# Kernel optimization log

Hardware: AMD Instinct MI355X
Metric: run time of the kernel (lower is better)

Reference implementation:

```python
import jax, jax.numpy as jnp
import numpy as np

D_MODEL = 1024
N_HEADS = 16
D_K = D_MODEL // N_HEADS
ROPE_BASE = 10000.0


def _rope_tables(seq_len, dim, dtype=jnp.float32):
    # standard rotary: inv_freq over even dims, angles broadcast over positions
    inv_freq = 1.0 / (ROPE_BASE ** (jnp.arange(0, dim, 2, dtype=jnp.float32) / dim))
    t = jnp.arange(seq_len, dtype=jnp.float32)
    freqs = jnp.outer(t, inv_freq)                  # [S, dim/2]
    emb = jnp.concatenate([freqs, freqs], axis=-1)   # [S, dim]
    return jnp.cos(emb).astype(dtype), jnp.sin(emb).astype(dtype)


def _rotate_half(x):
    x1, x2 = jnp.split(x, 2, axis=-1)
    return jnp.concatenate([-x2, x1], axis=-1)


def _apply_rope(x, cos, sin):
    # x: [B, H, S, d_k]; cos/sin: [S, d_k]
    return x * cos[None, None, :, :] + _rotate_half(x) * sin[None, None, :, :]


def setup_inputs() -> dict:
    key = jax.random.key(0)
    k1, k2, k3 = jax.random.split(key, 3)
    x = jax.random.normal(k1, (2, 2048, D_MODEL), dtype=jnp.float32)
    # torch Linear weights are [out, in]; store pre-transposed for x @ W
    scale = 1.0 / np.sqrt(D_MODEL)
    W_qkv = jax.random.normal(k2, (D_MODEL, 3 * D_MODEL), dtype=jnp.float32) * scale
    W_o = jax.random.normal(k3, (D_MODEL, D_MODEL), dtype=jnp.float32) * scale
    return {"x": x, "W_qkv": W_qkv, "W_o": W_o}


def reference(x, W_qkv, W_o):
    B, S, D = x.shape
    # fused QKV projection, then split into heads: [3, B, H, S, d_k]
    qkv = (x @ W_qkv).reshape(B, S, 3, N_HEADS, D_K).transpose(2, 0, 3, 1, 4)
    q, k, v = qkv[0], qkv[1], qkv[2]
    cos, sin = _rope_tables(S, D_K, x.dtype)
    q = _apply_rope(q, cos, sin)
    k = _apply_rope(k, cos, sin)
    # causal scaled dot-product attention (eval: dropout_p = 0)
    scores = jnp.einsum("bhqd,bhkd->bhqk", q, k) / jnp.sqrt(jnp.asarray(D_K, x.dtype))
    causal = jnp.tril(jnp.ones((S, S), dtype=bool))
    scores = jnp.where(causal[None, None], scores, jnp.asarray(-jnp.inf, x.dtype))
    attn = jax.nn.softmax(scores, axis=-1)
    out = jnp.einsum("bhqk,bhkd->bhqd", attn, v)          # [B, H, S, d_k]
    out = out.transpose(0, 2, 1, 3).reshape(B, S, D)       # [B, S, D]
    return out @ W_o
```

## Files before the change

kernel.cpp:

```cpp
#include <hip/hip_runtime.h>
#include <math.h>

#define B_ 2
#define S_ 2048
#define D_ 1024
#define H_ 16
#define DK_ 64
#define M_ (B_ * S_)
#define N3_ (3 * D_)

typedef __bf16 bf16;
typedef bf16 bf16x4 __attribute__((ext_vector_type(4)));
typedef bf16 bf16x8 __attribute__((ext_vector_type(8)));
typedef float f32x4 __attribute__((ext_vector_type(4)));
typedef short shortx4 __attribute__((ext_vector_type(4)));

#define GLL16(g, l)                                                     \
  __builtin_amdgcn_global_load_lds(                                     \
      (const __attribute__((address_space(1))) void*)(g),               \
      (__attribute__((address_space(3))) void*)(l), 16, 0, 0)


__global__ __launch_bounds__(256) void prep_k(
    const float* __restrict__ x, const float* __restrict__ Wqkv,
    const float* __restrict__ Wo, bf16* __restrict__ xb,
    bf16* __restrict__ Wqkv_bt, bf16* __restrict__ Wo_bt) {
  const int bx = blockIdx.x;
  if (bx < 4096) {
    int i = bx * 256 + threadIdx.x;
    float4 v = ((const float4*)x)[i];
    bf16x4 o = {(bf16)v.x, (bf16)v.y, (bf16)v.z, (bf16)v.w};
    ((bf16x4*)xb)[i] = o;
    return;
  }
  __shared__ float t[32][33];
  const float* src;
  bf16* dst;
  int R, C, cx, cy;
  if (bx < 4096 + 3072) {
    int b2 = bx - 4096;
    src = Wqkv; dst = Wqkv_bt; R = D_; C = N3_;
    cx = b2 % 96; cy = b2 / 96;
  } else {
    int b2 = bx - 7168;
    src = Wo; dst = Wo_bt; R = D_; C = D_;
    cx = b2 & 31; cy = b2 >> 5;
  }
  int r0 = cy * 32, c0 = cx * 32;
  int tx = threadIdx.x & 31, ty = threadIdx.x >> 5;
#pragma unroll
  for (int rr = 0; rr < 32; rr += 8)
    t[ty + rr][tx] = src[(size_t)(r0 + ty + rr) * C + c0 + tx];
  __syncthreads();
#pragma unroll
  for (int rr = 0; rr < 32; rr += 8)
    dst[(size_t)(c0 + ty + rr) * R + r0 + tx] = (bf16)t[tx][ty + rr];
}

#define GEMM_KLOOP(A, Bt, KDIM)                                              \
  __shared__ bf16 As[128 * 32];                                              \
  __shared__ bf16 Bs[128 * 32];                                              \
  const int tid = threadIdx.x;                                               \
  const int wave = tid >> 6, lane = tid & 63;                                \
  const int l15 = lane & 15, quad = lane >> 4;                               \
  const int wr = wave >> 1, wc = wave & 1;                                   \
  const int row0 = blockIdx.y * 128, col0 = blockIdx.x * 128;                \
  const int srow = (wave * 128 + lane) >> 2;                      \
  const int skc8 = (lane & 3) * 8;                                           \
  f32x4 acc[4][4] = {};                                                      \
  for (int k0 = 0; k0 < KDIM; k0 += 32) {                                    \
    __syncthreads();                                                         \
    _Pragma("unroll") for (int j = 0; j < 2; ++j) {                          \
      GLL16(A + (size_t)(row0 + srow + j * 16) * KDIM + k0 + skc8,           \
            &As[(wave * 128 + j * 64) * 8]);                                 \
      GLL16(Bt + (size_t)(col0 + srow + j * 16) * KDIM + k0 + skc8,          \
            &Bs[(wave * 128 + j * 64) * 8]);                                 \
    }                                                                        \
    __syncthreads();                                                         \
    bf16x8 af[4], bfr[4];                                                    \
    _Pragma("unroll") for (int i = 0; i < 4; ++i)                            \
        af[i] = *(const bf16x8*)&As[(wr * 64 + i * 16 + l15) * 32 + quad * 8]; \
    _Pragma("unroll") for (int t = 0; t < 4; ++t)                            \
        bfr[t] = *(const bf16x8*)&Bs[(wc * 64 + t * 16 + l15) * 32 + quad * 8]; \
    _Pragma("unroll") for (int i = 0; i < 4; ++i)                            \
        _Pragma("unroll") for (int t = 0; t < 4; ++t)                        \
            acc[i][t] = __builtin_amdgcn_mfma_f32_16x16x32_bf16(             \
                af[i], bfr[t], acc[i][t], 0, 0, 0);                          \
  }

__global__ __launch_bounds__(256) void gemm_qkv_mfma(
    const bf16* __restrict__ A, const bf16* __restrict__ Bt,
    bf16* __restrict__ Qb, bf16* __restrict__ Kb, bf16* __restrict__ VTb) {
  __shared__ bf16 Ct[4][32 * 72];
  GEMM_KLOOP(A, Bt, 1024)

  const int nb = col0 + wc * 64;
  const int which = nb >> 10;
  const int h = (nb >> 6) & 15;
  const float qsc = (which == 0) ? 0.125f : 1.0f;
  float freq[2];
#pragma unroll
  for (int t = 0; t < 2; ++t)
    freq[t] = exp2f((float)(t * 16 + l15) * -0.4152410118609203f);

  bf16* W = Ct[wave];
  const int mbase0 = row0 + wr * 64;
  const int bb = mbase0 >> 11;

#pragma unroll
  for (int ih = 0; ih < 2; ++ih) {
    __syncthreads();
    if (which == 2) {
#pragma unroll
      for (int i2 = 0; i2 < 2; ++i2) {
        int i = ih * 2 + i2;
#pragma unroll
        for (int r = 0; r < 4; ++r) {
          int sl = i2 * 16 + quad * 4 + r;
#pragma unroll
          for (int t = 0; t < 4; ++t)
            W[(t * 16 + l15) * 36 + sl] = (bf16)acc[i][t][r];
        }
      }
    } else {
#pragma unroll
      for (int i2 = 0; i2 < 2; ++i2) {
        int i = ih * 2 + i2;
#pragma unroll
        for (int r = 0; r < 4; ++r) {
          int ml = i2 * 16 + quad * 4 + r;
          int s = (mbase0 + i * 16 + quad * 4 + r) & (S_ - 1);
#pragma unroll
          for (int t = 0; t < 2; ++t) {
            float theta = (float)s * freq[t];
            float sn = __sinf(theta), cs = __cosf(theta);
            float x1 = acc[i][t][r], x2 = acc[i][t + 2][r];
            W[ml * 72 + t * 16 + l15] = (bf16)((x1 * cs - x2 * sn) * qsc);
            W[ml * 72 + t * 16 + l15 + 32] = (bf16)((x2 * cs + x1 * sn) * qsc);
          }
        }
      }
    }
    __syncthreads();
    const int s0 = (mbase0 + ih * 32) & (S_ - 1);
    if (which == 2) {
      bf16* vbase = VTb + ((size_t)(bb * H_ + h) * DK_) * (size_t)S_ + s0;
#pragma unroll
      for (int rr = 0; rr < 8; ++rr) {
        int d = rr * 8 + (lane >> 3);
        int c4 = (lane & 7) * 4;
        bf16x4 v = *(const bf16x4*)&W[d * 36 + c4];
        *(bf16x4*)(vbase + (size_t)d * S_ + c4) = v;
      }
    } else {
      bf16* basep = ((which == 0) ? Qb : Kb) +
                    (((size_t)(bb * H_ + h) * S_) + s0) * DK_;
#pragma unroll
      for (int rr = 0; rr < 4; ++rr) {
        int row = rr * 8 + (lane >> 3);
        int c8 = (lane & 7) * 8;
        bf16x8 v = *(const bf16x8*)&W[row * 72 + c8];
        *(bf16x8*)(basep + (size_t)row * DK_ + c8) = v;
      }
    }
  }
}

__global__ __launch_bounds__(256) void gemm_oproj_mfma(
    const bf16* __restrict__ A, const bf16* __restrict__ Bt,
    float* __restrict__ C) {
  GEMM_KLOOP(A, Bt, 1024)
#pragma unroll
  for (int i = 0; i < 4; ++i) {
#pragma unroll
    for (int r = 0; r < 4; ++r) {
      int m = row0 + wr * 64 + i * 16 + quad * 4 + r;
      float* dst = C + (size_t)m * D_ + col0 + wc * 64;
#pragma unroll
      for (int t = 0; t < 4; ++t) dst[t * 16 + l15] = acc[i][t][r];
    }
  }
}

__global__ __launch_bounds__(256) void attn_mfma(const bf16* __restrict__ Qb,
                                                 const bf16* __restrict__ Kb,
                                                 const bf16* __restrict__ VT,
                                                 bf16* __restrict__ Out) {
  __shared__ bf16 Ks[64 * 72];
  __shared__ bf16 Vs[64 * 68];

  const int tid = threadIdx.x;
  const int wave = tid >> 6, lane = tid & 63;
  const int l15 = lane & 15, quad = lane >> 4;

  const int bh = blockIdx.x & 31;
  const int q0 = (31 - (blockIdx.x >> 5)) * 64;
  const int qw = q0 + wave * 16;
  const size_t bh_off = (size_t)bh * (S_ * DK_);

  const bf16* qp = Qb + bh_off + (size_t)(qw + l15) * DK_ + quad * 8;
  bf16x8 qf0 = *(const bf16x8*)qp;
  bf16x8 qf1 = *(const bf16x8*)(qp + 32);

  f32x4 o_acc[4] = {};
  float lsum = 0.0f;

  for (int k0 = 0; k0 <= q0; k0 += 64) {
    __syncthreads();
#pragma unroll
    for (int it = 0; it < 2; ++it) {
      int e = tid + it * 256;
      int row = e >> 3, c8 = (e & 7) * 8;
      *(bf16x8*)&Ks[row * 72 + c8] =
          *(const bf16x8*)(Kb + bh_off + (size_t)(k0 + row) * DK_ + c8);
      *(bf16x8*)&Vs[row * 68 + c8] =
          *(const bf16x8*)(VT + bh_off + (size_t)row * S_ + k0 + c8);
    }
    __syncthreads();

    const bool dm = (k0 + 64 > qw);

    f32x4 st[4] = {};
#pragma unroll
    for (int t = 0; t < 4; ++t) {
      const bf16* kr = &Ks[(t * 16 + l15) * 72 + quad * 8];
      bf16x8 kf0 = *(const bf16x8*)kr;
      bf16x8 kf1 = *(const bf16x8*)(kr + 32);
      st[t] = __builtin_amdgcn_mfma_f32_16x16x32_bf16(kf0, qf0, st[t], 0, 0, 0);
      st[t] = __builtin_amdgcn_mfma_f32_16x16x32_bf16(kf1, qf1, st[t], 0, 0, 0);
    }

    bf16x4 pT[4];
    const int q = qw + l15;
#pragma unroll
    for (int t = 0; t < 4; ++t) {
#pragma unroll
      for (int r = 0; r < 4; ++r) {
        int key = k0 + t * 16 + quad * 4 + r;
        float p = __expf(st[t][r]);
        if (dm) p = (key <= q) ? p : 0.0f;
        lsum += p;
        pT[t][r] = (bf16)p;
      }
    }

#pragma unroll
    for (int u = 0; u < 4; ++u) {
#pragma unroll
      for (int t = 0; t < 4; ++t) {
        bf16x4 vf = *(const bf16x4*)&Vs[(u * 16 + l15) * 68 + t * 16 + quad * 4];
        o_acc[u] = __builtin_amdgcn_mfma_f32_16x16x16bf16_1k(
            __builtin_bit_cast(shortx4, pT[t]),
            __builtin_bit_cast(shortx4, vf), o_acc[u], 0, 0, 0);
      }
    }
  }

  const int b = bh >> 4, h = bh & 15;
  float l = lsum;
  l += __shfl_xor(l, 16, 64);
  l += __shfl_xor(l, 32, 64);
#pragma unroll
  for (int r = 0; r < 4; ++r) {
    float inv = 1.0f / __shfl(l, quad * 4 + r, 64);
    int q = qw + quad * 4 + r;
    bf16* op = Out + ((size_t)(b * S_ + q)) * D_ + h * DK_;
#pragma unroll
    for (int u = 0; u < 4; ++u)
      op[u * 16 + l15] = (bf16)(o_acc[u][r] * inv);
  }
}

extern "C" void kernel_launch(void* const* d_in, const int* in_sizes, int n_in,
                              void* d_out, int out_size, void* d_ws,
                              size_t ws_size, hipStream_t stream) {
  const float* x = (const float*)d_in[0];
  const float* Wqkv = (const float*)d_in[1];
  const float* Wo = (const float*)d_in[2];
  float* out = (float*)d_out;

  char* ws = (char*)d_ws;
  bf16* xb = (bf16*)(ws + 0);
  bf16* Wqkv_bt = (bf16*)(ws + (8u << 20));
  bf16* Wo_bt = (bf16*)(ws + (14u << 20));
  bf16* Qb = (bf16*)(ws + (16u << 20));
  bf16* Kb = (bf16*)(ws + (24u << 20));
  bf16* VTb = (bf16*)(ws + (32u << 20));
  bf16* AOb = (bf16*)(ws + (40u << 20));

  prep_k<<<4096 + 3072 + 1024, 256, 0, stream>>>(x, Wqkv, Wo, xb, Wqkv_bt,
                                                 Wo_bt);

  gemm_qkv_mfma<<<dim3(N3_ / 128, M_ / 128), 256, 0, stream>>>(xb, Wqkv_bt, Qb,
                                                               Kb, VTb);

  attn_mfma<<<B_ * H_ * (S_ / 64), 256, 0, stream>>>(Qb, Kb, VTb, AOb);

  gemm_oproj_mfma<<<dim3(D_ / 128, M_ / 128), 256, 0, stream>>>(AOb, Wo_bt, out);
}
```

Before: 176.9 us.

## Double attention query tile per block and fold log2e into Q scale

The attention kernel now gives each block 128 queries instead of 64, with each wave handling two 16-row query subtiles. Each K/V tile loaded into shared memory is therefore reused across twice as many queries, and the grid is halved. The Q scale now includes log2(e), so the softmax can use the native exp2 instruction instead of __expf. The trade-offs are higher register pressure, fewer blocks (lower occupancy and coarser causal load balance), and waves that skip fully masked tiles while still taking part in block syncs.

```diff
diff --git a/kernel.cpp b/kernel.cpp
--- a/kernel.cpp
+++ b/kernel.cpp
@@ -19,6 +19,8 @@
   __builtin_amdgcn_global_load_lds(                                     \
       (const __attribute__((address_space(1))) void*)(g),               \
       (__attribute__((address_space(3))) void*)(l), 16, 0, 0)
+
+#define QSCALE 0.1803368801111204f
 
 
 __global__ __launch_bounds__(256) void prep_k(
@@ -97,7 +99,7 @@
   const int nb = col0 + wc * 64;
   const int which = nb >> 10;
   const int h = (nb >> 6) & 15;
-  const float qsc = (which == 0) ? 0.125f : 1.0f;
+  const float qsc = (which == 0) ? QSCALE : 1.0f;
   float freq[2];
 #pragma unroll
   for (int t = 0; t < 2; ++t)
@@ -194,18 +196,23 @@
   const int l15 = lane & 15, quad = lane >> 4;
 
   const int bh = blockIdx.x & 31;
-  const int q0 = (31 - (blockIdx.x >> 5)) * 64;
-  const int qw = q0 + wave * 16;
+  const int q0 = (15 - (blockIdx.x >> 5)) * 128;
+  const int qw = q0 + wave * 32;
   const size_t bh_off = (size_t)bh * (S_ * DK_);
 
-  const bf16* qp = Qb + bh_off + (size_t)(qw + l15) * DK_ + quad * 8;
-  bf16x8 qf0 = *(const bf16x8*)qp;
-  bf16x8 qf1 = *(const bf16x8*)(qp + 32);
-
-  f32x4 o_acc[4] = {};
-  float lsum = 0.0f;
-
-  for (int k0 = 0; k0 <= q0; k0 += 64) {
+  bf16x8 qf[2][2];
+#pragma unroll
+  for (int s = 0; s < 2; ++s) {
+    const bf16* qp = Qb + bh_off + (size_t)(qw + 16 * s + l15) * DK_ + quad * 8;
+    qf[s][0] = *(const bf16x8*)qp;
+    qf[s][1] = *(const bf16x8*)(qp + 32);
+  }
+
+  f32x4 o_acc[2][4] = {};
+  float lsum[2] = {};
+
+  const int kn = q0 + 128;
+  for (int k0 = 0; k0 < kn; k0 += 64) {
     __syncthreads();
 #pragma unroll
     for (int it = 0; it < 2; ++it) {
@@ -218,29 +225,38 @@
     }
     __syncthreads();
 
+    if (k0 > qw + 31) continue;
     const bool dm = (k0 + 64 > qw);
 
-    f32x4 st[4] = {};
+    f32x4 st[2][4] = {};
 #pragma unroll
     for (int t = 0; t < 4; ++t) {
       const bf16* kr = &Ks[(t * 16 + l15) * 72 + quad * 8];
       bf16x8 kf0 = *(const bf16x8*)kr;
       bf16x8 kf1 = *(const bf16x8*)(kr + 32);
-      st[t] = __builtin_amdgcn_mfma_f32_16x16x32_bf16(kf0, qf0, st[t], 0, 0, 0);
-      st[t] = __builtin_amdgcn_mfma_f32_16x16x32_bf16(kf1, qf1, st[t], 0, 0, 0);
-    }
-
-    bf16x4 pT[4];
-    const int q = qw + l15;
-#pragma unroll
-    for (int t = 0; t < 4; ++t) {
-#pragma unroll
-      for (int r = 0; r < 4; ++r) {
-        int key = k0 + t * 16 + quad * 4 + r;
-        float p = __expf(st[t][r]);
-        if (dm) p = (key <= q) ? p : 0.0f;
-        lsum += p;
-        pT[t][r] = (bf16)p;
+#pragma unroll
+      for (int s = 0; s < 2; ++s) {
+        st[s][t] = __builtin_amdgcn_mfma_f32_16x16x32_bf16(kf0, qf[s][0],
+                                                           st[s][t], 0, 0, 0);
+        st[s][t] = __builtin_amdgcn_mfma_f32_16x16x32_bf16(kf1, qf[s][1],
+                                                           st[s][t], 0, 0, 0);
+      }
+    }
+
+    bf16x4 pT[2][4];
+#pragma unroll
+    for (int s = 0; s < 2; ++s) {
+      const int q = qw + 16 * s + l15;
+#pragma unroll
+      for (int t = 0; t < 4; ++t) {
+#pragma unroll
+        for (int r = 0; r < 4; ++r) {
+          int key = k0 + t * 16 + quad * 4 + r;
+          float p = __builtin_amdgcn_exp2f(st[s][t][r]);
+          if (dm) p = (key <= q) ? p : 0.0f;
+          lsum[s] += p;
+          pT[s][t][r] = (bf16)p;
+        }
       }
     }
 
@@ -249,25 +265,31 @@
 #pragma unroll
       for (int t = 0; t < 4; ++t) {
         bf16x4 vf = *(const bf16x4*)&Vs[(u * 16 + l15) * 68 + t * 16 + quad * 4];
-        o_acc[u] = __builtin_amdgcn_mfma_f32_16x16x16bf16_1k(
-            __builtin_bit_cast(shortx4, pT[t]),
-            __builtin_bit_cast(shortx4, vf), o_acc[u], 0, 0, 0);
+        shortx4 vs = __builtin_bit_cast(shortx4, vf);
+#pragma unroll
+        for (int s = 0; s < 2; ++s) {
+          o_acc[s][u] = __builtin_amdgcn_mfma_f32_16x16x16bf16_1k(
+              __builtin_bit_cast(shortx4, pT[s][t]), vs, o_acc[s][u], 0, 0, 0);
+        }
       }
     }
   }
 
   const int b = bh >> 4, h = bh & 15;
-  float l = lsum;
-  l += __shfl_xor(l, 16, 64);
-  l += __shfl_xor(l, 32, 64);
-#pragma unroll
-  for (int r = 0; r < 4; ++r) {
-    float inv = 1.0f / __shfl(l, quad * 4 + r, 64);
-    int q = qw + quad * 4 + r;
-    bf16* op = Out + ((size_t)(b * S_ + q)) * D_ + h * DK_;
-#pragma unroll
-    for (int u = 0; u < 4; ++u)
-      op[u * 16 + l15] = (bf16)(o_acc[u][r] * inv);
+#pragma unroll
+  for (int s = 0; s < 2; ++s) {
+    float l = lsum[s];
+    l += __shfl_xor(l, 16, 64);
+    l += __shfl_xor(l, 32, 64);
+#pragma unroll
+    for (int r = 0; r < 4; ++r) {
+      float inv = 1.0f / __shfl(l, quad * 4 + r, 64);
+      int q = qw + 16 * s + quad * 4 + r;
+      bf16* op = Out + ((size_t)(b * S_ + q)) * D_ + h * DK_;
+#pragma unroll
+      for (int u = 0; u < 4; ++u)
+        op[u * 16 + l15] = (bf16)(o_acc[s][u][r] * inv);
+    }
   }
 }
 
@@ -294,7 +316,7 @@
   gemm_qkv_mfma<<<dim3(N3_ / 128, M_ / 128), 256, 0, stream>>>(xb, Wqkv_bt, Qb,
                                                                Kb, VTb);
 
-  attn_mfma<<<B_ * H_ * (S_ / 64), 256, 0, stream>>>(Qb, Kb, VTb, AOb);
+  attn_mfma<<<B_ * H_ * (S_ / 128), 256, 0, stream>>>(Qb, Kb, VTb, AOb);
 
   gemm_oproj_mfma<<<dim3(D_ / 128, M_ / 128), 256, 0, stream>>>(AOb, Wo_bt, out);
 }
```

New measurement: 192.0 us. 1.09x slower.
